# Optimization experiments

Measured on AMD Instinct MI355X. Metric: run time of the kernel, lower is better.

Reference implementation:

```python
import jax, jax.numpy as jnp
import numpy as np

# Module constants (from init_kwargs)
NB_IN = 4          # num_blocks_in
NB_OUT = 8         # num_blocks_out
BS_IN = 128        # block_size_in (hard-coded in source)
NHID = 4096
BS_OUT = NHID // NB_OUT   # 512, also att_out
TOPK = 4
DK = 64            # d_k = d_v, n_head = 1


def _group_linear(x, w):
    # x: (B, n_blocks, d_in), w: (n_blocks, d_in, d_out) -> (B, n_blocks, d_out)
    return jnp.einsum('bnd,nde->bne', x, w)


def _attend(q, k, v):
    # single-head scaled dot-product attention
    attn = jax.nn.softmax(jnp.einsum('bqd,bkd->bqk', q, k) / jnp.sqrt(jnp.asarray(DK, q.dtype)), axis=-1)
    return jnp.einsum('bqk,bkd->bqd', attn, v), attn


def setup_inputs() -> dict:
    key = jax.random.key(0)
    ks = jax.random.split(key, 20)
    s = 0.02
    d = {
        'inp': jax.random.normal(ks[0], (1024, NB_IN * BS_IN), jnp.float32),
        'hx': jax.random.normal(ks[1], (1024, NHID), jnp.float32),
        'cx': jax.random.normal(ks[2], (1024, NHID), jnp.float32),
        # inp_att (residual=False): GroupLinear q/k/v + fc
        'ia_wq': jax.random.normal(ks[3], (NB_OUT, BS_OUT, DK), jnp.float32) * s,
        'ia_wk': jax.random.normal(ks[4], (NB_IN + 1, BS_IN, DK), jnp.float32) * s,
        'ia_wv': jax.random.normal(ks[5], (NB_IN + 1, BS_IN, DK), jnp.float32) * s,
        'ia_fc_w': jax.random.normal(ks[6], (DK, BS_OUT), jnp.float32) * s,
        'ia_fc_b': jnp.zeros((BS_OUT,), jnp.float32),
        # mha (residual=True, gated)
        'mha_wq': jax.random.normal(ks[7], (NB_OUT, BS_OUT, DK), jnp.float32) * s,
        'mha_wk': jax.random.normal(ks[8], (NB_OUT, BS_OUT, DK), jnp.float32) * s,
        'mha_wv': jax.random.normal(ks[9], (NB_OUT, BS_OUT, DK), jnp.float32) * s,
        'mha_fc_w': jax.random.normal(ks[10], (DK, BS_OUT), jnp.float32) * s,
        'mha_fc_b': jnp.zeros((BS_OUT,), jnp.float32),
        'mha_gate_w': jax.random.normal(ks[11], (DK, BS_OUT), jnp.float32) * s,
        'mha_gate_b': jnp.zeros((BS_OUT,), jnp.float32),
        # block-diagonal LSTM (BlockLSTM after blockify_params): per-block LSTMCell
        'w_ih': jax.random.normal(ks[12], (NB_OUT, BS_OUT, 4 * BS_OUT), jnp.float32) * s,
        'w_hh': jax.random.normal(ks[13], (NB_OUT, BS_OUT, 4 * BS_OUT), jnp.float32) * s,
        'b_ih': jnp.zeros((NB_OUT, 4 * BS_OUT), jnp.float32),
        'b_hh': jnp.zeros((NB_OUT, 4 * BS_OUT), jnp.float32),
    }
    return d


def _forward(inp, hx, cx, ia_wq, ia_wk, ia_wv, ia_fc_w, ia_fc_b,
             mha_wq, mha_wk, mha_wv, mha_fc_w, mha_fc_b, mha_gate_w, mha_gate_b,
             w_ih, w_hh, b_ih, b_hh):
    B = inp.shape[0]
    # --- input attention (inp_att) ---
    x = inp.reshape(B, NB_IN, BS_IN)
    x = jnp.concatenate([x, jnp.zeros_like(x[:, :1])], axis=1)        # append null block -> (B, NB_IN+1, BS_IN)
    hb = hx.reshape(B, NB_OUT, BS_OUT)
    q = _group_linear(hb, ia_wq)                                      # (B, NB_OUT, DK)
    k = _group_linear(x, ia_wk)
    v = _group_linear(x, ia_wv)
    o, iatt = _attend(q, k, v)                                        # o:(B,NB_OUT,DK), iatt:(B,NB_OUT,NB_IN+1)
    inp_use = (o @ ia_fc_w + ia_fc_b).reshape(B, NB_OUT * BS_OUT)     # residual=False path

    # --- top-k block selection mask (detached) ---
    score = iatt[:, :, 0]                                             # (B, NB_OUT)
    thr = jax.lax.top_k(score, TOPK)[0][:, -1]                        # k-th largest per sample
    mask_blk = (score > thr[:, None] - 0.01).astype(hx.dtype)         # (B, NB_OUT)
    mask = jnp.broadcast_to(mask_blk[:, :, None], (B, NB_OUT, BS_OUT)).reshape(B, NHID)
    mask = jax.lax.stop_gradient(mask)

    # --- block-diagonal LSTM update ---
    xb = inp_use.reshape(B, NB_OUT, BS_OUT)
    cb = cx.reshape(B, NB_OUT, BS_OUT)
    gates = (jnp.einsum('bkd,kdg->bkg', xb, w_ih) + b_ih
             + jnp.einsum('bkd,kdg->bkg', hb, w_hh) + b_hh)           # (B, NB_OUT, 4*BS_OUT)
    i_g, f_g, g_g, o_g = jnp.split(gates, 4, axis=-1)
    c_new = jax.nn.sigmoid(f_g) * cb + jax.nn.sigmoid(i_g) * jnp.tanh(g_g)
    h_new = jax.nn.sigmoid(o_g) * jnp.tanh(c_new)                     # (B, NB_OUT, BS_OUT)
    cx_new = c_new.reshape(B, NHID)

    # --- inter-block attention (step_att, residual + gate) ---
    residual = h_new
    q2 = _group_linear(h_new, mha_wq)
    k2 = _group_linear(h_new, mha_wk)
    v2 = _group_linear(h_new, mha_wv)
    o2, _ = _attend(q2, k2, v2)                                       # (B, NB_OUT, DK)
    out = o2 @ mha_fc_w + mha_fc_b
    gate = jax.nn.sigmoid(o2 @ mha_gate_w + mha_gate_b)
    hx_new = (residual + gate * jnp.tanh(out)).reshape(B, NHID)

    # --- masked blend of old / new states ---
    hx_out = mask * hx_new + (1.0 - mask) * hx
    cx_out = mask * cx_new + (1.0 - mask) * cx
    return hx_out, cx_out, mask


def reference(inp, hx, cx, ia_wq, ia_wk, ia_wv, ia_fc_w, ia_fc_b,
              mha_wq, mha_wk, mha_wv, mha_fc_w, mha_fc_b, mha_gate_w, mha_gate_b,
              w_ih, w_hh, b_ih, b_hh):
    return _forward(inp, hx, cx, ia_wq, ia_wk, ia_wv, ia_fc_w, ia_fc_b,
                    mha_wq, mha_wk, mha_wv, mha_fc_w, mha_fc_b, mha_gate_w, mha_gate_b,
                    w_ih, w_hh, b_ih, b_hh)
```

## Files before the change

### kernel.cpp

```cpp
#include <hip/hip_runtime.h>
#include <hip/hip_bf16.h>

#define B_    1024
#define NHID_ 4096
#define NBO   8
#define BSO   512
#define DK_   64

typedef __bf16 bf16;
typedef __bf16 bf16x2 __attribute__((ext_vector_type(2)));
typedef __bf16 bf16x4 __attribute__((ext_vector_type(4)));
typedef __bf16 bf16x8 __attribute__((ext_vector_type(8)));
typedef float  f32x4  __attribute__((ext_vector_type(4)));

__device__ __forceinline__ float sigf(float x){
    float e = __expf(-x);
    return __builtin_amdgcn_rcpf(1.0f + e);
}
__device__ __forceinline__ float ftanh(float x){
    float e = __expf(2.0f*x);
    return 1.0f - 2.0f*__builtin_amdgcn_rcpf(e + 1.0f);
}

__device__ __forceinline__ void gload16(const void* g, void* lds){
// ... 115 lines not shown
        int z  = bid>>8;
        int n = z>>1, which = z&1;
        const float* src = (which ? w_hh : w_ih) + (size_t)n*512*2048;
        #pragma unroll
        for (int it=0; it<4; ++it){
            int idx = t + it*256;
            int r = idx>>4, c4 = (idx&15)*4;
            *(float4*)&tile[r][c4] = *(const float4*)&src[(size_t)(k0+r)*2048 + c0 + c4];
        }
        __syncthreads();
        #pragma unroll
        for (int it=0; it<2; ++it){
            int idx = t + it*256;
            int c = idx>>3, r8 = (idx&7)*8;
            bf16x8 v;
            #pragma unroll
            for (int jj=0;jj<8;++jj) v[jj] = (bf16)tile[r8+jj][c];
            *(bf16x8*)&wT[((size_t)n*2048 + c0 + c)*1024 + which*512 + k0 + r8] = v;
        }
        return;
    }
    int gid = (bid-4096)*256 + t;
    if (gid < 1048576){
        float4 v = ((const float4*)hx)[gid];
        bf16x4 o; o.x=(bf16)v.x; o.y=(bf16)v.y; o.z=(bf16)v.z; o.w=(bf16)v.w;
        *(bf16x4*)&hb16[(size_t)gid*4] = o;
        return;
    }
    int e = gid - 1048576;
    if (e < 786432){
        int col = e >> 9, k = e & 511;
        int n = col / 192, c = col - n*192;
        int p = c >> 6, ee = c & 63;
        const float* s = (p==0) ? mha_wq : ((p==1) ? mha_wk : mha_wv);
        wqkvT[e] = (bf16)s[((size_t)n*512 + k)*64 + ee];
        return;
    }
    e -= 786432;
    if (e < 32768){
        int c = e>>6, k = e&63;
        iafcT[e] = (bf16)ia_fc_w[(size_t)k*512 + c];
        return;
    }
    e -= 32768;
    if (e < 65536){
        int cg = e>>6, k = e&63;
        int ct = cg>>6, j = cg&63;
        const float* s = (j<32) ? fc_w : gate_w;
        int col = ct*32 + (j&31);
        fcgT[e] = (bf16)s[(size_t)k*512 + col];
    }
}

__global__ __launch_bounds__(256) void k_score(const float* __restrict__ qbufH,
                                               const float* __restrict__ kbufH,
                                               const float* __restrict__ vbufH,
                                               const bf16* __restrict__ iafcT,
                                               const float* __restrict__ ia_fc_b,
                                               bf16* __restrict__ xb16,
                                               float* __restrict__ maskb,
                                               float* __restrict__ mask_out)
{
    int t = threadIdx.x, sb = t>>6, ts = t&63;
    int b = blockIdx.x*4 + sb;
    __shared__ float q_s[4][512];
    __shared__ float k_s[4][256];
    __shared__ float v_s[4][256];
    __shared__ float at_s[4][40];
    __shared__ float sc_s[4][8];
    __shared__ float mb_s[4][8];
    __shared__ bf16 o_s[32][72];

    #pragma unroll
    for (int r=0;r<8;++r){
        int i = ts + r*64;
        q_s[sb][i] = qbufH[(size_t)b*512 + i] + qbufH[(size_t)(B_+b)*512 + i];
    }
    #pragma unroll
    for (int r=0;r<4;++r){
        int i = ts + r*64;
        k_s[sb][i] = kbufH[(size_t)b*256 + i] + kbufH[(size_t)(B_+b)*256 + i];
        v_s[sb][i] = vbufH[(size_t)b*256 + i] + vbufH[(size_t)(B_+b)*256 + i];
    }
    __syncthreads();
    {
        int n = ts>>3, g = ts&7;
        const float* q = &q_s[sb][n*64];
        #pragma unroll
        for (int j=0;j<4;++j){
            const float* k = &k_s[sb][j*64];
            float s = 0.f;
            #pragma unroll
            for (int e=0;e<8;++e) s += q[g*8+e]*k[g*8+e];
            s += __shfl_xor(s, 1);
            s += __shfl_xor(s, 2);
            s += __shfl_xor(s, 4);
            if (g==0) at_s[sb][n*5+j] = s*0.125f;
        }
        if (g==1) at_s[sb][n*5+4] = 0.f;
    }
    __syncthreads();
    if (ts < 8){
        float m = at_s[sb][ts*5];
        for (int j=1;j<5;++j) m = fmaxf(m, at_s[sb][ts*5+j]);
        float ex[5]; float sum=0.f;
        for (int j=0;j<5;++j){ ex[j]=__expf(at_s[sb][ts*5+j]-m); sum+=ex[j]; }
        float inv = 1.f/sum;
        for (int j=0;j<5;++j) at_s[sb][ts*5+j] = ex[j]*inv;
        sc_s[sb][ts] = ex[0]*inv;
    }
    __syncthreads();
    if (ts == 0){
        float s[8];
        for (int nn=0;nn<8;++nn) s[nn] = sc_s[sb][nn];
        for (int ii=1;ii<8;++ii){ float key=s[ii]; int jj=ii-1;
            while(jj>=0 && s[jj]<key){ s[jj+1]=s[jj]; --jj; } s[jj+1]=key; }
        float thr = s[3]-0.01f;
        for (int nn=0;nn<8;++nn) mb_s[sb][nn] = (sc_s[sb][nn] > thr) ? 1.0f : 0.0f;
    }
    __syncthreads();
    #pragma unroll
    for (int r=0;r<8;++r){
        float s = 0.f;
        #pragma unroll
        for (int j=0;j<4;++j) s += at_s[sb][r*5+j]*v_s[sb][j*64+ts];
        o_s[sb*8+r][ts] = (bf16)s;
    }
    if (ts < 8) maskb[b*8+ts] = mb_s[sb][ts];
    float4* mo = (float4*)(mask_out + (size_t)b*4096);
    #pragma unroll
    for (int r=0;r<16;++r){
        int i4 = ts + r*64;
        float m = mb_s[sb][i4>>7];
        float4 mv; mv.x=m; mv.y=m; mv.z=m; mv.w=m;
        mo[i4] = mv;
    }
    __syncthreads();
    {
        int w = t>>6, l = t&63, quad = l>>4, l16 = l&15;
        int wm = w&1, wd = w>>1;
        bf16x8 a0 = *(const bf16x8*)&o_s[wm*16 + l16][quad*8];
        bf16x8 a1 = *(const bf16x8*)&o_s[wm*16 + l16][32 + quad*8];
        f32x4 zero = {0.f,0.f,0.f,0.f};
        #pragma unroll
        for (int nt=0; nt<16; ++nt){
            int cg = wd*256 + nt*16 + l16;
            bf16x8 b0 = *(const bf16x8*)&iafcT[(size_t)cg*64 + quad*8];
            bf16x8 b1 = *(const bf16x8*)&iafcT[(size_t)cg*64 + 32 + quad*8];
            f32x4 acc = __builtin_amdgcn_mfma_f32_16x16x32_bf16(a0, b0, zero, 0,0,0);
            acc = __builtin_amdgcn_mfma_f32_16x16x32_bf16(a1, b1, acc, 0,0,0);
            float bias = ia_fc_b[cg];
            #pragma unroll
            for (int v=0; v<4; ++v){
                int rm = wm*16 + quad*4 + v;
                int bb = blockIdx.x*4 + (rm>>3), nn = rm&7;
                xb16[(size_t)bb*4096 + nn*512 + cg] = (bf16)(acc[v] + bias);
            }
        }
    }
}

__global__ __launch_bounds__(256,2) void k_lstm(
    const bf16* __restrict__ xb16, const bf16* __restrict__ hb16,
    const bf16* __restrict__ wT, const float* __restrict__ b_ih,
    const float* __restrict__ b_hh, const float* __restrict__ cx,
    const float* __restrict__ maskb,
    float* __restrict__ cx_out, bf16* __restrict__ hn16)
{
    int bid = blockIdx.x;
    int n  = bid & 7;
    int i  = bid >> 3;
    int mt = i & 7, ct = i >> 3;
    int b0 = mt*128, d0 = ct*64;

    int t = threadIdx.x;
    int w = t >> 6, l = t & 63;
    int wm = w & 1, wg = w >> 1;
    int quad = l >> 4, l16 = l & 15;

    __shared__ __align__(16) bf16 lds[3*12288];

    int GA0 = (w*2)*64 + l, GA1 = GA0 + 64;
    int rA0 = GA0>>2,       rA1 = GA1>>2;
    int kA0 = (GA0&3) ^ ((rA0>>1)&3);
    int kA1 = (GA1&3) ^ ((rA1>>1)&3);
    const bf16* xbP0 = xb16 + (size_t)(b0+rA0)*4096 + n*512 + kA0*8;
    const bf16* xbP1 = xb16 + (size_t)(b0+rA1)*4096 + n*512 + kA1*8;
    const bf16* hbP0 = hb16 + (size_t)(b0+rA0)*4096 + n*512 + kA0*8;
    const bf16* hbP1 = hb16 + (size_t)(b0+rA1)*4096 + n*512 + kA1*8;

    const bf16* wbn = wT + (size_t)n*2048*1024;
    int GB0 = (w*4)*64 + l, GB1 = GB0+64, GB2 = GB0+128, GB3 = GB0+192;
    int vc0 = GB0>>2, vc1 = GB1>>2, vc2 = GB2>>2, vc3 = GB3>>2;
    int kB0 = (GB0&3) ^ ((vc0>>1)&3);
    int kB1 = (GB1&3) ^ ((vc1>>1)&3);
    int kB2 = (GB2&3) ^ ((vc2>>1)&3);
    int kB3 = (GB3&3) ^ ((vc3>>1)&3);
    const bf16* wP0 = wbn + (size_t)((vc0>>6)*512 + d0 + (vc0&63))*1024 + kB0*8;
    const bf16* wP1 = wbn + (size_t)((vc1>>6)*512 + d0 + (vc1&63))*1024 + kB1*8;
    const bf16* wP2 = wbn + (size_t)((vc2>>6)*512 + d0 + (vc2&63))*1024 + kB2*8;
    const bf16* wP3 = wbn + (size_t)((vc3>>6)*512 + d0 + (vc3&63))*1024 + kB3*8;

    int offA[4], offB[8];
    #pragma unroll
    for (int m=0;m<4;++m){ int R = wm*64 + m*16 + l16; offA[m] = (R*4 + (quad ^ ((R>>1)&3)))*8; }
    #pragma unroll
    for (int nf=0;nf<8;++nf){ int C = wg*128 + nf*16 + l16; offB[nf] = 4096 + (C*4 + (quad ^ ((C>>1)&3)))*8; }

    auto stA = [&](int buf, int kt){
        const bf16* s0 = (kt<16 ? xbP0 : hbP0) + (kt&15)*32;
        const bf16* s1 = (kt<16 ? xbP1 : hbP1) + (kt&15)*32;
        bf16* dst = &lds[buf*12288 + (w*2)*512];
        gload16(s0, dst);
        gload16(s1, dst + 512);
    };
    auto stB01 = [&](int buf, int kt){
        bf16* dst = &lds[buf*12288 + 4096 + (w*4)*512];
        gload16(wP0 + (size_t)kt*32, dst);
        gload16(wP1 + (size_t)kt*32, dst + 512);
    };
    auto stB23 = [&](int buf, int kt){
        bf16* dst = &lds[buf*12288 + 4096 + (w*4)*512];
        gload16(wP2 + (size_t)kt*32, dst + 1024);
        gload16(wP3 + (size_t)kt*32, dst + 1536);
    };

    f32x4 zero = {0.f,0.f,0.f,0.f};
    f32x4 acc[4][8];
    #pragma unroll
    for (int m=0;m<4;++m)
        #pragma unroll
        for (int nf=0;nf<8;++nf) acc[m][nf] = zero;

    stA(0,0); stB01(0,0); stB23(0,0);
    stA(1,1); stB01(1,1); stB23(1,1);
    WAITVM(6);
    sbar();

    int buf = 0, pbuf = 2;
    #pragma unroll 1
    for (int kt=0; kt<32; ++kt){
        const bf16* base = &lds[buf*12288];
        bf16x8 av[4], bv[4];

        if (kt < 30){ stA(pbuf, kt+2); stB01(pbuf, kt+2); }
        #pragma unroll
        for (int m=0;m<4;++m) av[m] = *(const bf16x8*)&base[offA[m]];
        #pragma unroll
        for (int nf=0;nf<4;++nf) bv[nf] = *(const bf16x8*)&base[offB[nf]];
        __builtin_amdgcn_s_setprio(1);
        #pragma unroll
        for (int m=0;m<4;++m)
            #pragma unroll
            for (int nf=0;nf<4;++nf)
                acc[m][nf] = __builtin_amdgcn_mfma_f32_16x16x32_bf16(av[m], bv[nf], acc[m][nf], 0,0,0);
        __builtin_amdgcn_s_setprio(0);
        sbar();

        if (kt < 30) stB23(pbuf, kt+2);
        #pragma unroll
        for (int nf=0;nf<4;++nf) bv[nf] = *(const bf16x8*)&base[offB[4+nf]];
        __builtin_amdgcn_s_setprio(1);
        #pragma unroll
        for (int m=0;m<4;++m)
            #pragma unroll
            for (int nf=0;nf<4;++nf)
                acc[m][4+nf] = __builtin_amdgcn_mfma_f32_16x16x32_bf16(av[m], bv[nf], acc[m][4+nf], 0,0,0);
        __builtin_amdgcn_s_setprio(0);
        if (kt < 30) { WAITVM(6); } else { WAITVM(0); }
        sbar();
        pbuf = buf; buf = (buf==2) ? 0 : buf+1;
    }

    float* gbuf = (float*)lds;
    const int GP = 260;
    int dl_t = t & 63;
    int i_t  = t >> 6;
    int d = d0 + dl_t;
    float bi  = b_ih[n*2048 +        d] + b_hh[n*2048 +        d];
    float bff = b_ih[n*2048 +  512 + d] + b_hh[n*2048 +  512 + d];
    float bg  = b_ih[n*2048 + 1024 + d] + b_hh[n*2048 + 1024 + d];
    float bo  = b_ih[n*2048 + 1536 + d] + b_hh[n*2048 + 1536 + d];

    #pragma unroll
    for (int c=0; c<2; ++c){
        if (wm == c){
            #pragma unroll
            for (int mm=0; mm<4; ++mm)
                #pragma unroll
                for (int nf=0; nf<8; ++nf)
                    #pragma unroll
                    for (int v=0; v<4; ++v)
                        gbuf[(mm*16 + quad*4 + v)*GP + wg*128 + nf*16 + l16] = acc[mm][nf][v];
        }
        __syncthreads();
        #pragma unroll
        for (int r=0; r<16; ++r){
            int row_l = i_t*16 + r;
            int row_g = b0 + c*64 + row_l;
            float gi = gbuf[row_l*GP +       dl_t] + bi;
            float gf = gbuf[row_l*GP +  64 + dl_t] + bff;
            float gg = gbuf[row_l*GP + 128 + dl_t] + bg;
            float go = gbuf[row_l*GP + 192 + dl_t] + bo;
            size_t gidx = (size_t)row_g*4096 + n*512 + d;
            float cb = cx[gidx];
            float cn = sigf(gf)*cb + sigf(gi)*ftanh(gg);
            float hn = sigf(go)*ftanh(cn);
            float mk = maskb[row_g*8 + n];
            cx_out[gidx] = (mk != 0.f) ? cn : cb;
            hn16[gidx]   = (bf16)hn;
        }
        __syncthreads();
    }
}

__global__ __launch_bounds__(256) void k_proj64(const bf16* __restrict__ hn16,
                                                const bf16* __restrict__ wqkvT,
                                                float* __restrict__ qkv2)
{
    int b0 = blockIdx.x*64, n = blockIdx.y, ct = blockIdx.z;
    int t = threadIdx.x, w = t>>6, l = t&63, quad = l>>4, l16 = l&15;
    int wm = w&1, wd = w>>1;
    __shared__ bf16 A_s[2][256*8];
    __shared__ bf16 B_s[2][256*8];
    f32x4 zero = {0.f,0.f,0.f,0.f};
    f32x4 acc[2][2] = {{zero,zero},{zero,zero}};
    const bf16* ab = hn16 + (size_t)n*512;
    const bf16* wb = wqkvT + ((size_t)n*192 + ct*64)*512;

    auto stage = [&](int buf, int k0){
        int row = t>>2, ss = t&3;
        int seg = ss ^ ((row>>1)&3);
        gload16(ab + (size_t)(b0+row)*4096 + k0 + seg*8, &A_s[buf][(w*64)*8]);
        gload16(wb + (size_t)row*512      + k0 + seg*8, &B_s[buf][(w*64)*8]);
    };

    stage(0, 0);
    for (int it=0; it<16; ++it){
        __syncthreads();
        if (it < 15) stage((it+1)&1, (it+1)*32);
        int buf = it&1;
        bf16x8 a[2], bb[2];
        #pragma unroll
        for (int r=0;r<2;++r){
            int row = wm*32 + r*16 + l16;
            int slot = row*4 + (quad ^ ((row>>1)&3));
            a[r] = *(const bf16x8*)&A_s[buf][slot*8];
        }
        #pragma unroll
        for (int c=0;c<2;++c){
            int col = wd*32 + c*16 + l16;
            int slot = col*4 + (quad ^ ((col>>1)&3));
            bb[c] = *(const bf16x8*)&B_s[buf][slot*8];
        }
        #pragma unroll
        for (int r=0;r<2;++r)
            #pragma unroll
            for (int c=0;c<2;++c)
                acc[r][c] = __builtin_amdgcn_mfma_f32_16x16x32_bf16(a[r], bb[c], acc[r][c], 0,0,0);
    }
    #pragma unroll
    for (int c=0;c<2;++c){
        int col = ct*64 + wd*32 + c*16 + l16;
        #pragma unroll
        for (int r=0;r<2;++r)
            #pragma unroll
            for (int v=0;v<4;++v){
                int row = b0 + wm*32 + r*16 + quad*4 + v;
                qkv2[(size_t)row*1536 + n*192 + col] = acc[r][c][v];
            }
    }
}

__global__ __launch_bounds__(256) void k_att2fc(const float* __restrict__ qkv2,
                                                const bf16* __restrict__ fcgT,
                                                const float* __restrict__ fc_b,
                                                const float* __restrict__ gate_b,
                                                const bf16* __restrict__ hn16,
                                                const float* __restrict__ hx,
                                                const float* __restrict__ maskb,
                                                float* __restrict__ hx_out)
{
    int t = threadIdx.x, sb = t>>6, ts = t&63;
    int b = blockIdx.x*4 + sb;
    __shared__ float q_s[4][512];
    __shared__ float k_s[4][512];
    __shared__ float v_s[4][512];
    __shared__ float at_s[4][64];
    __shared__ bf16 o_s[32][72];
    #pragma unroll
    for (int r=0;r<8;++r){
        int i = ts + r*64;
        int n = i>>6, e = i&63;
        const float* src = qkv2 + (size_t)b*1536 + n*192;
        q_s[sb][i] = src[e];
        k_s[sb][i] = src[64+e];
        v_s[sb][i] = src[128+e];
    }
    __syncthreads();
    {
        int n = ts>>3, g = ts&7;
        const float* q = &q_s[sb][n*64];
        #pragma unroll
        for (int j=0;j<8;++j){
            const float* k = &k_s[sb][j*64];
            float s = 0.f;
            #pragma unroll
            for (int e=0;e<8;++e) s += q[g*8+e]*k[g*8+e];
            s += __shfl_xor(s, 1);
            s += __shfl_xor(s, 2);
            s += __shfl_xor(s, 4);
            if (g==0) at_s[sb][n*8+j] = s*0.125f;
        }
    }
    __syncthreads();
    if (ts < 8){
        float m = at_s[sb][ts*8];
        for (int j=1;j<8;++j) m = fmaxf(m, at_s[sb][ts*8+j]);
        float ex[8]; float sum=0.f;
        for (int j=0;j<8;++j){ ex[j]=__expf(at_s[sb][ts*8+j]-m); sum+=ex[j]; }
        float inv = 1.f/sum;
        for (int j=0;j<8;++j) at_s[sb][ts*8+j] = ex[j]*inv;
    }
    __syncthreads();
    #pragma unroll
    for (int r=0;r<8;++r){
        float s = 0.f;
        #pragma unroll
        for (int j=0;j<8;++j) s += at_s[sb][r*8+j]*v_s[sb][j*64+ts];
        o_s[sb*8+r][ts] = (bf16)s;
    }
    __syncthreads();
    {
        int w = t>>6, l = t&63, quad = l>>4, l16 = l&15;
        int wm = w&1, wd = w>>1;
        bf16x8 a0 = *(const bf16x8*)&o_s[wm*16 + l16][quad*8];
        bf16x8 a1 = *(const bf16x8*)&o_s[wm*16 + l16][32 + quad*8];
        f32x4 zero = {0.f,0.f,0.f,0.f};
        f32x4 acc[32];
        #pragma unroll
        for (int nt=0; nt<32; ++nt){
            int cg = wd*512 + nt*16 + l16;
            bf16x8 b0 = *(const bf16x8*)&fcgT[(size_t)cg*64 + quad*8];
            bf16x8 b1 = *(const bf16x8*)&fcgT[(size_t)cg*64 + 32 + quad*8];
            acc[nt] = __builtin_amdgcn_mfma_f32_16x16x32_bf16(a0, b0, zero, 0,0,0);
            acc[nt] = __builtin_amdgcn_mfma_f32_16x16x32_bf16(a1, b1, acc[nt], 0,0,0);
        }
        #pragma unroll
        for (int ctl=0; ctl<8; ++ctl){
            #pragma unroll
            for (int s=0; s<2; ++s){
                int d = (wd*8+ctl)*32 + s*16 + l16;
                float fb = fc_b[d], gb = gate_b[d];
                f32x4 fa = acc[ctl*4+s], ga = acc[ctl*4+2+s];
                #pragma unroll
                for (int v=0; v<4; ++v){
                    int rm = wm*16 + quad*4 + v;
                    int bb = blockIdx.x*4 + (rm>>3), nn = rm&7;
                    size_t idx = (size_t)bb*4096 + nn*512 + d;
                    float f = fa[v] + fb;
                    float g = ga[v] + gb;
                    float hnv = (float)hn16[idx];
                    float mk = maskb[bb*8+nn];
                    hx_out[idx] = (mk != 0.f) ? (hnv + sigf(g)*ftanh(f)) : hx[idx];
                }
            }
        }
    }
}

extern "C" void kernel_launch(void* const* d_in, const int* in_sizes, int n_in,
                              void* d_out, int out_size, void* d_ws, size_t ws_size,
                              hipStream_t stream)
{
    const float* inp       = (const float*)d_in[0];
    const float* hx        = (const float*)d_in[1];
    const float* cx        = (const float*)d_in[2];
    const float* ia_wq     = (const float*)d_in[3];
    const float* ia_wk     = (const float*)d_in[4];
    const float* ia_wv     = (const float*)d_in[5];
    const float* ia_fc_w   = (const float*)d_in[6];
    const float* ia_fc_b   = (const float*)d_in[7];
    const float* mha_wq    = (const float*)d_in[8];
    const float* mha_wk    = (const float*)d_in[9];
    const float* mha_wv    = (const float*)d_in[10];
    const float* mha_fc_w  = (const float*)d_in[11];
    const float* mha_fc_b  = (const float*)d_in[12];
    const float* mha_gate_w= (const float*)d_in[13];
    const float* mha_gate_b= (const float*)d_in[14];
    const float* w_ih      = (const float*)d_in[15];
    const float* w_hh      = (const float*)d_in[16];
    const float* b_ih      = (const float*)d_in[17];
    const float* b_hh      = (const float*)d_in[18];

    float* hx_out  = (float*)d_out;
    float* cx_out  = hx_out + (size_t)B_*NHID_;
    float* mask_out= cx_out + (size_t)B_*NHID_;

    char* p = (char*)d_ws;
    bf16* wT     = (bf16*)p;               p += (size_t)8*2048*1024*2;
    bf16* hb16   = (bf16*)p;               p += (size_t)B_*NHID_*2;
    bf16* xb16   = (bf16*)p;               p += (size_t)B_*NHID_*2;
    bf16* hn16   = (bf16*)p;               p += (size_t)B_*NHID_*2;
    bf16* wqkvT  = (bf16*)p;               p += (size_t)8*192*512*2;
    bf16* iafcT  = (bf16*)p;               p += (size_t)512*64*2;
    bf16* fcgT   = (bf16*)p;               p += (size_t)1024*64*2;
    float* qbufH = (float*)p;              p += (size_t)2*B_*512*4;
    float* kbufH = (float*)p;              p += (size_t)2*B_*256*4;
    float* vbufH = (float*)p;              p += (size_t)2*B_*256*4;
    float* qkv2  = (float*)p;              p += (size_t)B_*1536*4;
    float* maskb = (float*)p;              p += (size_t)B_*8*4;

    hipLaunchKernelGGL(k_prepqkv, dim3(12416), dim3(256), 0, stream,
                       w_ih, w_hh, hx, inp, ia_wq, ia_wk, ia_wv,
                       mha_wq, mha_wk, mha_wv, ia_fc_w, mha_fc_w, mha_gate_w,
                       wT, hb16, wqkvT, iafcT, fcgT, qbufH, kbufH, vbufH);
    hipLaunchKernelGGL(k_score, dim3(256), dim3(256), 0, stream,
                       qbufH, kbufH, vbufH, iafcT, ia_fc_b, xb16, maskb, mask_out);
    hipLaunchKernelGGL(k_lstm, dim3(512), dim3(256), 0, stream,
                       xb16, hb16, wT, b_ih, b_hh, cx, maskb, cx_out, hn16);
    hipLaunchKernelGGL(k_proj64, dim3(16,8,3), dim3(256), 0, stream, hn16, wqkvT, qkv2);
    hipLaunchKernelGGL(k_att2fc, dim3(256), dim3(256), 0, stream,
                       qkv2, fcgT, mha_fc_b, mha_gate_b, hn16, hx, maskb, hx_out);
}
```

Before: 284.3 us.

## Retile LSTM GEMM to 256x256 tiles with 4-stage buffering; shrink attention blocks

The LSTM gate GEMM now uses 512-thread blocks computing 256 rows by 256 gate columns, with a 4-deep LDS ring buffer replacing the 3-stage one. This halves the grid and increases reuse of weight and activation tiles. The two attention kernels now run one batch row per 64-thread block on 1024 blocks, padding the MFMA A tile with zero rows and writing only the valid half. The changes aim to cut global traffic in the LSTM GEMM and improve occupancy and latency hiding in the small kernels. They add padded MFMA work, more LDS per block, and more register pressure.

```diff
diff --git a/kernel.cpp b/kernel.cpp
--- a/kernel.cpp
+++ b/kernel.cpp
@@ -191,115 +191,120 @@
     }
 }
 
-__global__ __launch_bounds__(256) void k_score(const float* __restrict__ qbufH,
-                                               const float* __restrict__ kbufH,
-                                               const float* __restrict__ vbufH,
-                                               const bf16* __restrict__ iafcT,
-                                               const float* __restrict__ ia_fc_b,
-                                               bf16* __restrict__ xb16,
-                                               float* __restrict__ maskb,
-                                               float* __restrict__ mask_out)
+__global__ __launch_bounds__(64) void k_score(const float* __restrict__ qbufH,
+                                              const float* __restrict__ kbufH,
+                                              const float* __restrict__ vbufH,
+                                              const bf16* __restrict__ iafcT,
+                                              const float* __restrict__ ia_fc_b,
+                                              bf16* __restrict__ xb16,
+                                              float* __restrict__ maskb,
+                                              float* __restrict__ mask_out)
 {
-    int t = threadIdx.x, sb = t>>6, ts = t&63;
-    int b = blockIdx.x*4 + sb;
-    __shared__ float q_s[4][512];
-    __shared__ float k_s[4][256];
-    __shared__ float v_s[4][256];
-    __shared__ float at_s[4][40];
-    __shared__ float sc_s[4][8];
-    __shared__ float mb_s[4][8];
-    __shared__ bf16 o_s[32][72];
+    int ts = threadIdx.x;
+    int b = blockIdx.x;
+    __shared__ float q_s[512];
+    __shared__ float k_s[256];
+    __shared__ float v_s[256];
+    __shared__ float at_s[40];
+    __shared__ float sc_s[8];
+    __shared__ float mb_s[8];
+    __shared__ bf16 o_s[16][72];
 
     #pragma unroll
     for (int r=0;r<8;++r){
         int i = ts + r*64;
-        q_s[sb][i] = qbufH[(size_t)b*512 + i] + qbufH[(size_t)(B_+b)*512 + i];
+        q_s[i] = qbufH[(size_t)b*512 + i] + qbufH[(size_t)(B_+b)*512 + i];
     }
     #pragma unroll
     for (int r=0;r<4;++r){
         int i = ts + r*64;
-        k_s[sb][i] = kbufH[(size_t)b*256 + i] + kbufH[(size_t)(B_+b)*256 + i];
-        v_s[sb][i] = vbufH[(size_t)b*256 + i] + vbufH[(size_t)(B_+b)*256 + i];
+        k_s[i] = kbufH[(size_t)b*256 + i] + kbufH[(size_t)(B_+b)*256 + i];
+        v_s[i] = vbufH[(size_t)b*256 + i] + vbufH[(size_t)(B_+b)*256 + i];
     }
     __syncthreads();
     {
         int n = ts>>3, g = ts&7;
-        const float* q = &q_s[sb][n*64];
+        const float* q = &q_s[n*64];
         #pragma unroll
         for (int j=0;j<4;++j){
-            const float* k = &k_s[sb][j*64];
+            const float* k = &k_s[j*64];
             float s = 0.f;
             #pragma unroll
             for (int e=0;e<8;++e) s += q[g*8+e]*k[g*8+e];
             s += __shfl_xor(s, 1);
             s += __shfl_xor(s, 2);
             s += __shfl_xor(s, 4);
-            if (g==0) at_s[sb][n*5+j] = s*0.125f;
-        }
-        if (g==1) at_s[sb][n*5+4] = 0.f;
+            if (g==0) at_s[n*5+j] = s*0.125f;
+        }
+        if (g==1) at_s[n*5+4] = 0.f;
     }
     __syncthreads();
     if (ts < 8){
-        float m = at_s[sb][ts*5];
-        for (int j=1;j<5;++j) m = fmaxf(m, at_s[sb][ts*5+j]);
+        float m = at_s[ts*5];
+        for (int j=1;j<5;++j) m = fmaxf(m, at_s[ts*5+j]);
         float ex[5]; float sum=0.f;
-        for (int j=0;j<5;++j){ ex[j]=__expf(at_s[sb][ts*5+j]-m); sum+=ex[j]; }
+        for (int j=0;j<5;++j){ ex[j]=__expf(at_s[ts*5+j]-m); sum+=ex[j]; }
         float inv = 1.f/sum;
-        for (int j=0;j<5;++j) at_s[sb][ts*5+j] = ex[j]*inv;
-        sc_s[sb][ts] = ex[0]*inv;
+        for (int j=0;j<5;++j) at_s[ts*5+j] = ex[j]*inv;
+        sc_s[ts] = ex[0]*inv;
     }
     __syncthreads();
     if (ts == 0){
         float s[8];
-        for (int nn=0;nn<8;++nn) s[nn] = sc_s[sb][nn];
+        for (int nn=0;nn<8;++nn) s[nn] = sc_s[nn];
         for (int ii=1;ii<8;++ii){ float key=s[ii]; int jj=ii-1;
             while(jj>=0 && s[jj]<key){ s[jj+1]=s[jj]; --jj; } s[jj+1]=key; }
         float thr = s[3]-0.01f;
-        for (int nn=0;nn<8;++nn) mb_s[sb][nn] = (sc_s[sb][nn] > thr) ? 1.0f : 0.0f;
+        for (int nn=0;nn<8;++nn) mb_s[nn] = (sc_s[nn] > thr) ? 1.0f : 0.0f;
     }
     __syncthreads();
     #pragma unroll
     for (int r=0;r<8;++r){
         float s = 0.f;
         #pragma unroll
-        for (int j=0;j<4;++j) s += at_s[sb][r*5+j]*v_s[sb][j*64+ts];
-        o_s[sb*8+r][ts] = (bf16)s;
-    }
-    if (ts < 8) maskb[b*8+ts] = mb_s[sb][ts];
+        for (int j=0;j<4;++j) s += at_s[r*5+j]*v_s[j*64+ts];
+        o_s[r][ts] = (bf16)s;
+    }
+    {
+        int zr = 8 + (ts>>3), zc = (ts&7)*8;
+        bf16x8 zz = {};
+        *(bf16x8*)&o_s[zr][zc] = zz;
+    }
+    if (ts < 8) maskb[b*8+ts] = mb_s[ts];
     float4* mo = (float4*)(mask_out + (size_t)b*4096);
     #pragma unroll
     for (int r=0;r<16;++r){
         int i4 = ts + r*64;
-        float m = mb_s[sb][i4>>7];
+        float m = mb_s[i4>>7];
         float4 mv; mv.x=m; mv.y=m; mv.z=m; mv.w=m;
         mo[i4] = mv;
     }
     __syncthreads();
     {
-        int w = t>>6, l = t&63, quad = l>>4, l16 = l&15;
-        int wm = w&1, wd = w>>1;
-        bf16x8 a0 = *(const bf16x8*)&o_s[wm*16 + l16][quad*8];
-        bf16x8 a1 = *(const bf16x8*)&o_s[wm*16 + l16][32 + quad*8];
+        int quad = ts>>4, l16 = ts&15;
+        bf16x8 a0 = *(const bf16x8*)&o_s[l16][quad*8];
+        bf16x8 a1 = *(const bf16x8*)&o_s[l16][32 + quad*8];
         f32x4 zero = {0.f,0.f,0.f,0.f};
         #pragma unroll
-        for (int nt=0; nt<16; ++nt){
-            int cg = wd*256 + nt*16 + l16;
+        for (int nt=0; nt<32; ++nt){
+            int cg = nt*16 + l16;
             bf16x8 b0 = *(const bf16x8*)&iafcT[(size_t)cg*64 + quad*8];
             bf16x8 b1 = *(const bf16x8*)&iafcT[(size_t)cg*64 + 32 + quad*8];
             f32x4 acc = __builtin_amdgcn_mfma_f32_16x16x32_bf16(a0, b0, zero, 0,0,0);
             acc = __builtin_amdgcn_mfma_f32_16x16x32_bf16(a1, b1, acc, 0,0,0);
-            float bias = ia_fc_b[cg];
-            #pragma unroll
-            for (int v=0; v<4; ++v){
-                int rm = wm*16 + quad*4 + v;
-                int bb = blockIdx.x*4 + (rm>>3), nn = rm&7;
-                xb16[(size_t)bb*4096 + nn*512 + cg] = (bf16)(acc[v] + bias);
-            }
-        }
-    }
-}
-
-__global__ __launch_bounds__(256,2) void k_lstm(
+            if (quad < 2){
+                float bias = ia_fc_b[cg];
+                #pragma unroll
+                for (int v=0; v<4; ++v){
+                    int rm = quad*4 + v;
+                    xb16[(size_t)b*4096 + rm*512 + cg] = (bf16)(acc[v] + bias);
+                }
+            }
+        }
+    }
+}
+
+__global__ __launch_bounds__(512,2) void k_lstm(
     const bf16* __restrict__ xb16, const bf16* __restrict__ hb16,
     const bf16* __restrict__ wT, const float* __restrict__ b_ih,
     const float* __restrict__ b_hh, const float* __restrict__ cx,
@@ -309,84 +314,75 @@
     int bid = blockIdx.x;
     int n  = bid & 7;
     int i  = bid >> 3;
-    int mt = i & 7, ct = i >> 3;
-    int b0 = mt*128, d0 = ct*64;
+    int mt = i & 3, nt = i >> 2;
+    int b0 = mt*256, d0 = nt*64;
 
     int t = threadIdx.x;
     int w = t >> 6, l = t & 63;
-    int wm = w & 1, wg = w >> 1;
+    int wr = w >> 2, wc = w & 3;
     int quad = l >> 4, l16 = l & 15;
 
-    __shared__ __align__(16) bf16 lds[3*12288];
-
-    int GA0 = (w*2)*64 + l, GA1 = GA0 + 64;
-    int rA0 = GA0>>2,       rA1 = GA1>>2;
-    int kA0 = (GA0&3) ^ ((rA0>>1)&3);
-    int kA1 = (GA1&3) ^ ((rA1>>1)&3);
-    const bf16* xbP0 = xb16 + (size_t)(b0+rA0)*4096 + n*512 + kA0*8;
-    const bf16* xbP1 = xb16 + (size_t)(b0+rA1)*4096 + n*512 + kA1*8;
-    const bf16* hbP0 = hb16 + (size_t)(b0+rA0)*4096 + n*512 + kA0*8;
-    const bf16* hbP1 = hb16 + (size_t)(b0+rA1)*4096 + n*512 + kA1*8;
-
-    const bf16* wbn = wT + (size_t)n*2048*1024;
-    int GB0 = (w*4)*64 + l, GB1 = GB0+64, GB2 = GB0+128, GB3 = GB0+192;
-    int vc0 = GB0>>2, vc1 = GB1>>2, vc2 = GB2>>2, vc3 = GB3>>2;
-    int kB0 = (GB0&3) ^ ((vc0>>1)&3);
-    int kB1 = (GB1&3) ^ ((vc1>>1)&3);
-    int kB2 = (GB2&3) ^ ((vc2>>1)&3);
-    int kB3 = (GB3&3) ^ ((vc3>>1)&3);
-    const bf16* wP0 = wbn + (size_t)((vc0>>6)*512 + d0 + (vc0&63))*1024 + kB0*8;
-    const bf16* wP1 = wbn + (size_t)((vc1>>6)*512 + d0 + (vc1&63))*1024 + kB1*8;
-    const bf16* wP2 = wbn + (size_t)((vc2>>6)*512 + d0 + (vc2&63))*1024 + kB2*8;
-    const bf16* wP3 = wbn + (size_t)((vc3>>6)*512 + d0 + (vc3&63))*1024 + kB3*8;
-
-    int offA[4], offB[8];
-    #pragma unroll
-    for (int m=0;m<4;++m){ int R = wm*64 + m*16 + l16; offA[m] = (R*4 + (quad ^ ((R>>1)&3)))*8; }
-    #pragma unroll
-    for (int nf=0;nf<8;++nf){ int C = wg*128 + nf*16 + l16; offB[nf] = 4096 + (C*4 + (quad ^ ((C>>1)&3)))*8; }
+    __shared__ __align__(16) bf16 lds[4*16384];
+
+    int G0 = t;
+    int rowA0 = G0>>2, rowA1 = rowA0 + 128;
+    int ksA0 = (G0&3) ^ ((rowA0>>1)&3);
+    int ksA1 = (G0&3) ^ ((rowA1>>1)&3);
+    const bf16* xbP0 = xb16 + (size_t)(b0+rowA0)*4096 + n*512 + ksA0*8;
+    const bf16* hbP0 = hb16 + (size_t)(b0+rowA0)*4096 + n*512 + ksA0*8;
+    const bf16* xbP1 = xb16 + (size_t)(b0+rowA1)*4096 + n*512 + ksA1*8;
+    const bf16* hbP1 = hb16 + (size_t)(b0+rowA1)*4096 + n*512 + ksA1*8;
+
+    int vc0 = G0>>2, vc1 = vc0 + 128;
+    int ksB0 = (G0&3) ^ ((vc0>>1)&3);
+    int ksB1 = (G0&3) ^ ((vc1>>1)&3);
+    const bf16* wb = wT + (size_t)n*2048*1024;
+    const bf16* wP0 = wb + (size_t)((vc0>>6)*512 + d0 + (vc0&63))*1024 + ksB0*8;
+    const bf16* wP1 = wb + (size_t)((vc1>>6)*512 + d0 + (vc1&63))*1024 + ksB1*8;
+
+    int offA[8], offB[4];
+    #pragma unroll
+    for (int m=0;m<8;++m){ int R = wr*128 + m*16 + l16; offA[m] = (R*4 + (quad ^ ((R>>1)&3)))*8; }
+    #pragma unroll
+    for (int nf=0;nf<4;++nf){ int C = wc*64 + nf*16 + l16; offB[nf] = (C*4 + (quad ^ ((C>>1)&3)))*8; }
 
     auto stA = [&](int buf, int kt){
         const bf16* s0 = (kt<16 ? xbP0 : hbP0) + (kt&15)*32;
         const bf16* s1 = (kt<16 ? xbP1 : hbP1) + (kt&15)*32;
-        bf16* dst = &lds[buf*12288 + (w*2)*512];
+        bf16* dst = &lds[buf*16384 + w*512];
         gload16(s0, dst);
-        gload16(s1, dst + 512);
+        gload16(s1, dst + 4096);
     };
-    auto stB01 = [&](int buf, int kt){
-        bf16* dst = &lds[buf*12288 + 4096 + (w*4)*512];
-        gload16(wP0 + (size_t)kt*32, dst);
-        gload16(wP1 + (size_t)kt*32, dst + 512);
+    auto stB = [&](int buf, int kt){
+        bf16* dst = &lds[buf*16384 + 8192 + w*512];
+        gload16(wP0 + kt*32, dst);
+        gload16(wP1 + kt*32, dst + 4096);
     };
-    auto stB23 = [&](int buf, int kt){
-        bf16* dst = &lds[buf*12288 + 4096 + (w*4)*512];
-        gload16(wP2 + (size_t)kt*32, dst + 1024);
-        gload16(wP3 + (size_t)kt*32, dst + 1536);
-    };
 
     f32x4 zero = {0.f,0.f,0.f,0.f};
-    f32x4 acc[4][8];
-    #pragma unroll
-    for (int m=0;m<4;++m)
-        #pragma unroll
-        for (int nf=0;nf<8;++nf) acc[m][nf] = zero;
-
-    stA(0,0); stB01(0,0); stB23(0,0);
-    stA(1,1); stB01(1,1); stB23(1,1);
-    WAITVM(6);
+    f32x4 acc[8][4];
+    #pragma unroll
+    for (int m=0;m<8;++m)
+        #pragma unroll
+        for (int nf=0;nf<4;++nf) acc[m][nf] = zero;
+
+    stA(0,0); stB(0,0);
+    stA(1,1); stB(1,1);
+    WAITVM(4);
     sbar();
 
-    int buf = 0, pbuf = 2;
-    #pragma unroll 1
+    #pragma unroll 2
     for (int kt=0; kt<32; ++kt){
-        const bf16* base = &lds[buf*12288];
+        int buf = kt & 3;
+        const bf16* Ab = &lds[buf*16384];
+        const bf16* Bb = Ab + 8192;
         bf16x8 av[4], bv[4];
 
-        if (kt < 30){ stA(pbuf, kt+2); stB01(pbuf, kt+2); }
-        #pragma unroll
-        for (int m=0;m<4;++m) av[m] = *(const bf16x8*)&base[offA[m]];
-        #pragma unroll
-        for (int nf=0;nf<4;++nf) bv[nf] = *(const bf16x8*)&base[offB[nf]];
+        if (kt < 30) stA((kt+2)&3, kt+2);
+        #pragma unroll
+        for (int m=0;m<4;++m) av[m] = *(const bf16x8*)&Ab[offA[m]];
+        #pragma unroll
+        for (int nf=0;nf<4;++nf) bv[nf] = *(const bf16x8*)&Bb[offB[nf]];
         __builtin_amdgcn_s_setprio(1);
         #pragma unroll
         for (int m=0;m<4;++m)
@@ -396,19 +392,18 @@
         __builtin_amdgcn_s_setprio(0);
         sbar();
 
-        if (kt < 30) stB23(pbuf, kt+2);
-        #pragma unroll
-        for (int nf=0;nf<4;++nf) bv[nf] = *(const bf16x8*)&base[offB[4+nf]];
+        if (kt < 30) stB((kt+2)&3, kt+2);
+        #pragma unroll
+        for (int m=0;m<4;++m) av[m] = *(const bf16x8*)&Ab[offA[4+m]];
         __builtin_amdgcn_s_setprio(1);
         #pragma unroll
         for (int m=0;m<4;++m)
             #pragma unroll
             for (int nf=0;nf<4;++nf)
-                acc[m][4+nf] = __builtin_amdgcn_mfma_f32_16x16x32_bf16(av[m], bv[nf], acc[m][4+nf], 0,0,0);
+                acc[4+m][nf] = __builtin_amdgcn_mfma_f32_16x16x32_bf16(av[m], bv[nf], acc[4+m][nf], 0,0,0);
         __builtin_amdgcn_s_setprio(0);
-        if (kt < 30) { WAITVM(6); } else { WAITVM(0); }
+        if (kt < 30) { WAITVM(4); } else { WAITVM(0); }
         sbar();
-        pbuf = buf; buf = (buf==2) ? 0 : buf+1;
     }
 
     float* gbuf = (float*)lds;
@@ -422,20 +417,20 @@
     float bo  = b_ih[n*2048 + 1536 + d] + b_hh[n*2048 + 1536 + d];
 
     #pragma unroll
-    for (int c=0; c<2; ++c){
-        if (wm == c){
+    for (int c=0; c<4; ++c){
+        if (wr == (c>>1)){
             #pragma unroll
             for (int mm=0; mm<4; ++mm)
                 #pragma unroll
-                for (int nf=0; nf<8; ++nf)
+                for (int nf=0; nf<4; ++nf)
                     #pragma unroll
                     for (int v=0; v<4; ++v)
-                        gbuf[(mm*16 + quad*4 + v)*GP + wg*128 + nf*16 + l16] = acc[mm][nf][v];
+                        gbuf[(mm*16 + quad*4 + v)*GP + wc*64 + nf*16 + l16] = acc[(c&1)*4 + mm][nf][v];
         }
         __syncthreads();
         #pragma unroll
-        for (int r=0; r<16; ++r){
-            int row_l = i_t*16 + r;
+        for (int r=0; r<8; ++r){
+            int row_l = i_t*8 + r;
             int row_g = b0 + c*64 + row_l;
             float gi = gbuf[row_l*GP +       dl_t] + bi;
             float gf = gbuf[row_l*GP +  64 + dl_t] + bff;
@@ -511,97 +506,101 @@
     }
 }
 
-__global__ __launch_bounds__(256) void k_att2fc(const float* __restrict__ qkv2,
-                                                const bf16* __restrict__ fcgT,
-                                                const float* __restrict__ fc_b,
-                                                const float* __restrict__ gate_b,
-                                                const bf16* __restrict__ hn16,
-                                                const float* __restrict__ hx,
-                                                const float* __restrict__ maskb,
-                                                float* __restrict__ hx_out)
+__global__ __launch_bounds__(64) void k_att2fc(const float* __restrict__ qkv2,
+                                               const bf16* __restrict__ fcgT,
+                                               const float* __restrict__ fc_b,
+                                               const float* __restrict__ gate_b,
+                                               const bf16* __restrict__ hn16,
+                                               const float* __restrict__ hx,
+                                               const float* __restrict__ maskb,
+                                               float* __restrict__ hx_out)
 {
-    int t = threadIdx.x, sb = t>>6, ts = t&63;
-    int b = blockIdx.x*4 + sb;
-    __shared__ float q_s[4][512];
-    __shared__ float k_s[4][512];
-    __shared__ float v_s[4][512];
-    __shared__ float at_s[4][64];
-    __shared__ bf16 o_s[32][72];
+    int ts = threadIdx.x;
+    int b = blockIdx.x;
+    __shared__ float q_s[512];
+    __shared__ float k_s[512];
+    __shared__ float v_s[512];
+    __shared__ float at_s[64];
+    __shared__ bf16 o_s[16][72];
     #pragma unroll
     for (int r=0;r<8;++r){
         int i = ts + r*64;
         int n = i>>6, e = i&63;
         const float* src = qkv2 + (size_t)b*1536 + n*192;
-        q_s[sb][i] = src[e];
-        k_s[sb][i] = src[64+e];
-        v_s[sb][i] = src[128+e];
+        q_s[i] = src[e];
+        k_s[i] = src[64+e];
+        v_s[i] = src[128+e];
     }
     __syncthreads();
     {
         int n = ts>>3, g = ts&7;
-        const float* q = &q_s[sb][n*64];
+        const float* q = &q_s[n*64];
         #pragma unroll
         for (int j=0;j<8;++j){
-            const float* k = &k_s[sb][j*64];
+            const float* k = &k_s[j*64];
             float s = 0.f;
             #pragma unroll
             for (int e=0;e<8;++e) s += q[g*8+e]*k[g*8+e];
             s += __shfl_xor(s, 1);
             s += __shfl_xor(s, 2);
             s += __shfl_xor(s, 4);
-            if (g==0) at_s[sb][n*8+j] = s*0.125f;
+            if (g==0) at_s[n*8+j] = s*0.125f;
         }
     }
     __syncthreads();
     if (ts < 8){
-        float m = at_s[sb][ts*8];
-        for (int j=1;j<8;++j) m = fmaxf(m, at_s[sb][ts*8+j]);
+        float m = at_s[ts*8];
+        for (int j=1;j<8;++j) m = fmaxf(m, at_s[ts*8+j]);
         float ex[8]; float sum=0.f;
-        for (int j=0;j<8;++j){ ex[j]=__expf(at_s[sb][ts*8+j]-m); sum+=ex[j]; }
+        for (int j=0;j<8;++j){ ex[j]=__expf(at_s[ts*8+j]-m); sum+=ex[j]; }
         float inv = 1.f/sum;
-        for (int j=0;j<8;++j) at_s[sb][ts*8+j] = ex[j]*inv;
+        for (int j=0;j<8;++j) at_s[ts*8+j] = ex[j]*inv;
     }
     __syncthreads();
     #pragma unroll
     for (int r=0;r<8;++r){
         float s = 0.f;
         #pragma unroll
-        for (int j=0;j<8;++j) s += at_s[sb][r*8+j]*v_s[sb][j*64+ts];
-        o_s[sb*8+r][ts] = (bf16)s;
-    }
-    __syncthreads();
+        for (int j=0;j<8;++j) s += at_s[r*8+j]*v_s[j*64+ts];
+        o_s[r][ts] = (bf16)s;
+    }
     {
-        int w = t>>6, l = t&63, quad = l>>4, l16 = l&15;
-        int wm = w&1, wd = w>>1;
-        bf16x8 a0 = *(const bf16x8*)&o_s[wm*16 + l16][quad*8];
-        bf16x8 a1 = *(const bf16x8*)&o_s[wm*16 + l16][32 + quad*8];
+        int zr = 8 + (ts>>3), zc = (ts&7)*8;
+        bf16x8 zz = {};
+        *(bf16x8*)&o_s[zr][zc] = zz;
+    }
+    __syncthreads();
+    {
+        int quad = ts>>4, l16 = ts&15;
+        bf16x8 a0 = *(const bf16x8*)&o_s[l16][quad*8];
+        bf16x8 a1 = *(const bf16x8*)&o_s[l16][32 + quad*8];
         f32x4 zero = {0.f,0.f,0.f,0.f};
-        f32x4 acc[32];
-        #pragma unroll
-        for (int nt=0; nt<32; ++nt){
-            int cg = wd*512 + nt*16 + l16;
-            bf16x8 b0 = *(const bf16x8*)&fcgT[(size_t)cg*64 + quad*8];
-            bf16x8 b1 = *(const bf16x8*)&fcgT[(size_t)cg*64 + 32 + quad*8];
-            acc[nt] = __builtin_amdgcn_mfma_f32_16x16x32_bf16(a0, b0, zero, 0,0,0);
-            acc[nt] = __builtin_amdgcn_mfma_f32_16x16x32_bf16(a1, b1, acc[nt], 0,0,0);
-        }
-        #pragma unroll
-        for (int ctl=0; ctl<8; ++ctl){
-            #pragma unroll
-            for (int s=0; s<2; ++s){
-                int d = (wd*8+ctl)*32 + s*16 + l16;
-                float fb = fc_b[d], gb = gate_b[d];
-                f32x4 fa = acc[ctl*4+s], ga = acc[ctl*4+2+s];
+        #pragma unroll
+        for (int ct=0; ct<16; ++ct){
+            f32x4 accs[4];
+            #pragma unroll
+            for (int s4=0; s4<4; ++s4){
+                int cg = ct*64 + s4*16 + l16;
+                bf16x8 b0 = *(const bf16x8*)&fcgT[(size_t)cg*64 + quad*8];
+                bf16x8 b1 = *(const bf16x8*)&fcgT[(size_t)cg*64 + 32 + quad*8];
+                accs[s4] = __builtin_amdgcn_mfma_f32_16x16x32_bf16(a0, b0, zero, 0,0,0);
+                accs[s4] = __builtin_amdgcn_mfma_f32_16x16x32_bf16(a1, b1, accs[s4], 0,0,0);
+            }
+            if (quad < 2){
                 #pragma unroll
-                for (int v=0; v<4; ++v){
-                    int rm = wm*16 + quad*4 + v;
-                    int bb = blockIdx.x*4 + (rm>>3), nn = rm&7;
-                    size_t idx = (size_t)bb*4096 + nn*512 + d;
-                    float f = fa[v] + fb;
-                    float g = ga[v] + gb;
-                    float hnv = (float)hn16[idx];
-                    float mk = maskb[bb*8+nn];
-                    hx_out[idx] = (mk != 0.f) ? (hnv + sigf(g)*ftanh(f)) : hx[idx];
+                for (int s=0; s<2; ++s){
+                    int d = ct*32 + s*16 + l16;
+                    float fb = fc_b[d], gb = gate_b[d];
+                    #pragma unroll
+                    for (int v=0; v<4; ++v){
+                        int rm = quad*4 + v;
+                        size_t idx = (size_t)b*4096 + rm*512 + d;
+                        float f = accs[s][v]   + fb;
+                        float g = accs[2+s][v] + gb;
+                        float hnv = (float)hn16[idx];
+                        float mk = maskb[b*8+rm];
+                        hx_out[idx] = (mk != 0.f) ? (hnv + sigf(g)*ftanh(f)) : hx[idx];
+                    }
                 }
             }
         }
@@ -654,11 +653,11 @@
                        w_ih, w_hh, hx, inp, ia_wq, ia_wk, ia_wv,
                        mha_wq, mha_wk, mha_wv, ia_fc_w, mha_fc_w, mha_gate_w,
                        wT, hb16, wqkvT, iafcT, fcgT, qbufH, kbufH, vbufH);
-    hipLaunchKernelGGL(k_score, dim3(256), dim3(256), 0, stream,
+    hipLaunchKernelGGL(k_score, dim3(1024), dim3(64), 0, stream,
                        qbufH, kbufH, vbufH, iafcT, ia_fc_b, xb16, maskb, mask_out);
-    hipLaunchKernelGGL(k_lstm, dim3(512), dim3(256), 0, stream,
+    hipLaunchKernelGGL(k_lstm, dim3(256), dim3(512), 0, stream,
                        xb16, hb16, wT, b_ih, b_hh, cx, maskb, cx_out, hn16);
     hipLaunchKernelGGL(k_proj64, dim3(16,8,3), dim3(256), 0, stream, hn16, wqkvT, qkv2);
-    hipLaunchKernelGGL(k_att2fc, dim3(256), dim3(256), 0, stream,
+    hipLaunchKernelGGL(k_att2fc, dim3(1024), dim3(64), 0, stream,
                        qkv2, fcgT, mha_fc_b, mha_gate_b, hn16, hx, maskb, hx_out);
 }
```

After: 327.2 us. +15.1%, slower.

## Retile LSTM GEMM to 256x256 blocks with four-stage single-barrier pipeline

Applied to the files above, without the earlier changes.

The block-diagonal LSTM GEMM kernel moves from 256-thread blocks computing 128x256 tiles to 512-thread blocks computing 256x256 tiles, halving the grid to 256 blocks. The LDS ring grows from three to four stages, so each k-step needs only one barrier instead of two, and each wave now holds an 8x4 MFMA fragment grid. The aim is to raise data reuse per loaded A/B byte and cut synchronisation overhead. In exchange, LDS use rises to 128 KB per block, which likely allows only one block per CU. It also leaves a single wave of blocks with no tail balancing, and register pressure per thread goes up.

```diff
diff --git a/kernel.cpp b/kernel.cpp
--- a/kernel.cpp
+++ b/kernel.cpp
@@ -299,7 +299,7 @@
     }
 }
 
-__global__ __launch_bounds__(256,2) void k_lstm(
+__global__ __launch_bounds__(512,2) void k_lstm(
     const bf16* __restrict__ xb16, const bf16* __restrict__ hb16,
     const bf16* __restrict__ wT, const float* __restrict__ b_ih,
     const float* __restrict__ b_hh, const float* __restrict__ cx,
@@ -309,106 +309,87 @@
     int bid = blockIdx.x;
     int n  = bid & 7;
     int i  = bid >> 3;
-    int mt = i & 7, ct = i >> 3;
-    int b0 = mt*128, d0 = ct*64;
+    int mt = i & 3, nt = i >> 2;
+    int b0 = mt*256, d0 = nt*64;
 
     int t = threadIdx.x;
     int w = t >> 6, l = t & 63;
-    int wm = w & 1, wg = w >> 1;
+    int wr = w >> 2, wc = w & 3;
     int quad = l >> 4, l16 = l & 15;
 
-    __shared__ __align__(16) bf16 lds[3*12288];
-
-    int GA0 = (w*2)*64 + l, GA1 = GA0 + 64;
-    int rA0 = GA0>>2,       rA1 = GA1>>2;
-    int kA0 = (GA0&3) ^ ((rA0>>1)&3);
-    int kA1 = (GA1&3) ^ ((rA1>>1)&3);
-    const bf16* xbP0 = xb16 + (size_t)(b0+rA0)*4096 + n*512 + kA0*8;
-    const bf16* xbP1 = xb16 + (size_t)(b0+rA1)*4096 + n*512 + kA1*8;
-    const bf16* hbP0 = hb16 + (size_t)(b0+rA0)*4096 + n*512 + kA0*8;
-    const bf16* hbP1 = hb16 + (size_t)(b0+rA1)*4096 + n*512 + kA1*8;
-
-    const bf16* wbn = wT + (size_t)n*2048*1024;
-    int GB0 = (w*4)*64 + l, GB1 = GB0+64, GB2 = GB0+128, GB3 = GB0+192;
-    int vc0 = GB0>>2, vc1 = GB1>>2, vc2 = GB2>>2, vc3 = GB3>>2;
-    int kB0 = (GB0&3) ^ ((vc0>>1)&3);
-    int kB1 = (GB1&3) ^ ((vc1>>1)&3);
-    int kB2 = (GB2&3) ^ ((vc2>>1)&3);
-    int kB3 = (GB3&3) ^ ((vc3>>1)&3);
-    const bf16* wP0 = wbn + (size_t)((vc0>>6)*512 + d0 + (vc0&63))*1024 + kB0*8;
-    const bf16* wP1 = wbn + (size_t)((vc1>>6)*512 + d0 + (vc1&63))*1024 + kB1*8;
-    const bf16* wP2 = wbn + (size_t)((vc2>>6)*512 + d0 + (vc2&63))*1024 + kB2*8;
-    const bf16* wP3 = wbn + (size_t)((vc3>>6)*512 + d0 + (vc3&63))*1024 + kB3*8;
-
-    int offA[4], offB[8];
-    #pragma unroll
-    for (int m=0;m<4;++m){ int R = wm*64 + m*16 + l16; offA[m] = (R*4 + (quad ^ ((R>>1)&3)))*8; }
-    #pragma unroll
-    for (int nf=0;nf<8;++nf){ int C = wg*128 + nf*16 + l16; offB[nf] = 4096 + (C*4 + (quad ^ ((C>>1)&3)))*8; }
+    __shared__ __align__(16) bf16 lds[4*16384];
+
+    int G0 = t;
+    int rowA0 = G0>>2, rowA1 = rowA0 + 128;
+    int ksA0 = (G0&3) ^ ((rowA0>>1)&3);
+    int ksA1 = (G0&3) ^ ((rowA1>>1)&3);
+    const bf16* xbP0 = xb16 + (size_t)(b0+rowA0)*4096 + n*512 + ksA0*8;
+    const bf16* hbP0 = hb16 + (size_t)(b0+rowA0)*4096 + n*512 + ksA0*8;
+    const bf16* xbP1 = xb16 + (size_t)(b0+rowA1)*4096 + n*512 + ksA1*8;
+    const bf16* hbP1 = hb16 + (size_t)(b0+rowA1)*4096 + n*512 + ksA1*8;
+
+    int vc0 = G0>>2, vc1 = vc0 + 128;
+    int ksB0 = (G0&3) ^ ((vc0>>1)&3);
+    int ksB1 = (G0&3) ^ ((vc1>>1)&3);
+    const bf16* wb = wT + (size_t)n*2048*1024;
+    const bf16* wP0 = wb + (size_t)((vc0>>6)*512 + d0 + (vc0&63))*1024 + ksB0*8;
+    const bf16* wP1 = wb + (size_t)((vc1>>6)*512 + d0 + (vc1&63))*1024 + ksB1*8;
+
+    int offA[8], offB[4];
+    #pragma unroll
+    for (int m=0;m<8;++m){ int R = wr*128 + m*16 + l16; offA[m] = (R*4 + (quad ^ ((R>>1)&3)))*8; }
+    #pragma unroll
+    for (int nf=0;nf<4;++nf){ int C = wc*64 + nf*16 + l16; offB[nf] = (C*4 + (quad ^ ((C>>1)&3)))*8; }
 
     auto stA = [&](int buf, int kt){
         const bf16* s0 = (kt<16 ? xbP0 : hbP0) + (kt&15)*32;
         const bf16* s1 = (kt<16 ? xbP1 : hbP1) + (kt&15)*32;
-        bf16* dst = &lds[buf*12288 + (w*2)*512];
+        bf16* dst = &lds[buf*16384 + w*512];
         gload16(s0, dst);
-        gload16(s1, dst + 512);
+        gload16(s1, dst + 4096);
     };
-    auto stB01 = [&](int buf, int kt){
-        bf16* dst = &lds[buf*12288 + 4096 + (w*4)*512];
-        gload16(wP0 + (size_t)kt*32, dst);
-        gload16(wP1 + (size_t)kt*32, dst + 512);
+    auto stB = [&](int buf, int kt){
+        bf16* dst = &lds[buf*16384 + 8192 + w*512];
+        gload16(wP0 + kt*32, dst);
+        gload16(wP1 + kt*32, dst + 4096);
     };
-    auto stB23 = [&](int buf, int kt){
-        bf16* dst = &lds[buf*12288 + 4096 + (w*4)*512];
-        gload16(wP2 + (size_t)kt*32, dst + 1024);
-        gload16(wP3 + (size_t)kt*32, dst + 1536);
-    };
 
     f32x4 zero = {0.f,0.f,0.f,0.f};
-    f32x4 acc[4][8];
-    #pragma unroll
-    for (int m=0;m<4;++m)
-        #pragma unroll
-        for (int nf=0;nf<8;++nf) acc[m][nf] = zero;
-
-    stA(0,0); stB01(0,0); stB23(0,0);
-    stA(1,1); stB01(1,1); stB23(1,1);
-    WAITVM(6);
+    f32x4 acc[8][4];
+    #pragma unroll
+    for (int m=0;m<8;++m)
+        #pragma unroll
+        for (int nf=0;nf<4;++nf) acc[m][nf] = zero;
+
+    stA(0,0); stB(0,0);
+    stA(1,1); stB(1,1);
+    WAITVM(4);
     sbar();
 
-    int buf = 0, pbuf = 2;
-    #pragma unroll 1
+    #pragma unroll 2
     for (int kt=0; kt<32; ++kt){
-        const bf16* base = &lds[buf*12288];
-        bf16x8 av[4], bv[4];
-
-        if (kt < 30){ stA(pbuf, kt+2); stB01(pbuf, kt+2); }
-        #pragma unroll
-        for (int m=0;m<4;++m) av[m] = *(const bf16x8*)&base[offA[m]];
-        #pragma unroll
-        for (int nf=0;nf<4;++nf) bv[nf] = *(const bf16x8*)&base[offB[nf]];
+        int buf = kt & 3;
+        const bf16* Ab = &lds[buf*16384];
+        const bf16* Bb = Ab + 8192;
+
+        if (kt < 30){ stA((kt+2)&3, kt+2); stB((kt+2)&3, kt+2); }
+
+        bf16x8 av[8], bv[4];
+        #pragma unroll
+        for (int m=0;m<8;++m) av[m] = *(const bf16x8*)&Ab[offA[m]];
+        #pragma unroll
+        for (int nf=0;nf<4;++nf) bv[nf] = *(const bf16x8*)&Bb[offB[nf]];
+
         __builtin_amdgcn_s_setprio(1);
         #pragma unroll
-        for (int m=0;m<4;++m)
+        for (int m=0;m<8;++m)
             #pragma unroll
             for (int nf=0;nf<4;++nf)
                 acc[m][nf] = __builtin_amdgcn_mfma_f32_16x16x32_bf16(av[m], bv[nf], acc[m][nf], 0,0,0);
         __builtin_amdgcn_s_setprio(0);
+
+        if (kt < 30) { WAITVM(4); } else { WAITVM(0); }
         sbar();
-
-        if (kt < 30) stB23(pbuf, kt+2);
-        #pragma unroll
-        for (int nf=0;nf<4;++nf) bv[nf] = *(const bf16x8*)&base[offB[4+nf]];
-        __builtin_amdgcn_s_setprio(1);
-        #pragma unroll
-        for (int m=0;m<4;++m)
-            #pragma unroll
-            for (int nf=0;nf<4;++nf)
-                acc[m][4+nf] = __builtin_amdgcn_mfma_f32_16x16x32_bf16(av[m], bv[nf], acc[m][4+nf], 0,0,0);
-        __builtin_amdgcn_s_setprio(0);
-        if (kt < 30) { WAITVM(6); } else { WAITVM(0); }
-        sbar();
-        pbuf = buf; buf = (buf==2) ? 0 : buf+1;
     }
 
     float* gbuf = (float*)lds;
@@ -422,20 +403,20 @@
     float bo  = b_ih[n*2048 + 1536 + d] + b_hh[n*2048 + 1536 + d];
 
     #pragma unroll
-    for (int c=0; c<2; ++c){
-        if (wm == c){
+    for (int c=0; c<4; ++c){
+        if (wr == (c>>1)){
             #pragma unroll
             for (int mm=0; mm<4; ++mm)
                 #pragma unroll
-                for (int nf=0; nf<8; ++nf)
+                for (int nf=0; nf<4; ++nf)
                     #pragma unroll
                     for (int v=0; v<4; ++v)
-                        gbuf[(mm*16 + quad*4 + v)*GP + wg*128 + nf*16 + l16] = acc[mm][nf][v];
+                        gbuf[(mm*16 + quad*4 + v)*GP + wc*64 + nf*16 + l16] = acc[(c&1)*4 + mm][nf][v];
         }
         __syncthreads();
         #pragma unroll
-        for (int r=0; r<16; ++r){
-            int row_l = i_t*16 + r;
+        for (int r=0; r<8; ++r){
+            int row_l = i_t*8 + r;
             int row_g = b0 + c*64 + row_l;
             float gi = gbuf[row_l*GP +       dl_t] + bi;
             float gf = gbuf[row_l*GP +  64 + dl_t] + bff;
@@ -656,7 +637,7 @@
                        wT, hb16, wqkvT, iafcT, fcgT, qbufH, kbufH, vbufH);
     hipLaunchKernelGGL(k_score, dim3(256), dim3(256), 0, stream,
                        qbufH, kbufH, vbufH, iafcT, ia_fc_b, xb16, maskb, mask_out);
-    hipLaunchKernelGGL(k_lstm, dim3(512), dim3(256), 0, stream,
+    hipLaunchKernelGGL(k_lstm, dim3(256), dim3(512), 0, stream,
                        xb16, hb16, wT, b_ih, b_hh, cx, maskb, cx_out, hn16);
     hipLaunchKernelGGL(k_proj64, dim3(16,8,3), dim3(256), 0, stream, hn16, wqkvT, qkv2);
     hipLaunchKernelGGL(k_att2fc, dim3(256), dim3(256), 0, stream,
```

After: 280.9 us. About the same (-1.2%).
